# Kernel optimization log

Measured on AMD Instinct MI355X. Metric: run time of the kernel, lower is better.

Reference implementation:

```python
import math
import jax
import jax.numpy as jnp
import numpy as np

SEGMENT_SIZE = 2048   # w (init: segment_size)
DILATION_RATE = 4     # r (init: dilation_rate)
D_MODEL = 1024        # init: d_model


def _sparse_indices(n: int, w: int, r: int, head_idx: int) -> np.ndarray:
    """Static SparsifyIndices: per segment of size w, take tokens offset::r.
    Since r divides w, every segment yields exactly m=w//r indices (no -1 pad).
    Returns flat global token indices, shape (S*m,)."""
    S = n // w
    m = w // r
    off = head_idx % r
    seg_start = np.arange(S, dtype=np.int64)[:, None] * w      # (S,1)
    within = off + r * np.arange(m, dtype=np.int64)[None, :]   # (1,m)
    return (seg_start + within).reshape(-1)


def setup_inputs() -> dict:
    key = jax.random.key(0)
    x = jax.random.normal(key, (4, 8192, D_MODEL), dtype=jnp.float32)
    return {"x": x, "head_idx": 1}


def reference(x, head_idx):
    b, n0, d = x.shape
    w, r = SEGMENT_SIZE, DILATION_RATE
    pad = (-n0) % w
    if pad:
        x = jnp.pad(x, ((0, 0), (0, pad), (0, 0)))
    n = n0 + pad
    idx = _sparse_indices(n, w, r, int(head_idx))  # static, (S*m,)
    S, m = n // w, w // r

    # Gather dilated tokens per segment: (b, S, m, d)
    xg = x[:, idx, :].reshape(b, S, m, d)

    # Softmax attention within each sub-segment (q=k=v=xg)
    scores = jnp.einsum('bsid,bsjd->bsij', xg, xg) / math.sqrt(d)  # (b,S,m,m)
    probs = jax.nn.softmax(scores, axis=-1)
    att = jnp.einsum('bsij,bsjd->bsid', probs, xg).reshape(b, S * m, d)

    # MixOutputs: alpha-weighted scatter-add back to full sequence
    denoms = att.sum(-1)                                       # (b, S*m)
    denom_sums = jnp.zeros((b, n), x.dtype).at[:, idx].add(denoms)
    alphas = denoms / denom_sums[:, idx]                       # (b, S*m)
    out = jnp.zeros((b, n, d), x.dtype).at[:, idx, :].add(att * alphas[..., None])
    return out
```

## Files before the change

kernel.cpp:

```cpp
#include <hip/hip_runtime.h>
#include <hip/hip_bf16.h>


typedef __bf16 bf16_t;
typedef __bf16 bf16x8 __attribute__((ext_vector_type(8)));
typedef float floatx4 __attribute__((ext_vector_type(4)));

#define D_MODEL 1024
#define SEG_W   2048
#define RATE    4
#define M_SUB   512
#define NTOK    8192
#define NSEGT   16
#define XG_ELEMS ((long)NSEGT * M_SUB * D_MODEL)

__global__ __launch_bounds__(256) void gather_kernel(
    const float* __restrict__ x, const int* __restrict__ hidp,
    bf16_t* __restrict__ xg, bf16_t* __restrict__ xgT)
{
    const int off = ((hidp[0] % RATE) + RATE) % RATE;
    const int bid = blockIdx.x;
    const int seg = bid >> 7;
    const int rem = bid & 127;
    const int it  = rem >> 4;
    const int dt  = rem & 15;
    const int b   = seg >> 2, s = seg & 3;

    __shared__ ushort tile[64][65];

    const int t  = threadIdx.x;
    const int r  = t >> 2;
    const int cq = (t & 3) << 4;

    union U8 { bf16x8 v; ushort u[8]; };

    {
        const int  i   = it * 64 + r;
        const long tok = (long)s * SEG_W + off + 4L * i;
        const float* src = x + ((long)b * NTOK + tok) * D_MODEL + dt * 64 + cq;
        float4 f0 = ((const float4*)src)[0];
        float4 f1 = ((const float4*)src)[1];
        float4 f2 = ((const float4*)src)[2];
        float4 f3 = ((const float4*)src)[3];
        U8 lo, hi;
        lo.v[0]=(bf16_t)f0.x; lo.v[1]=(bf16_t)f0.y; lo.v[2]=(bf16_t)f0.z; lo.v[3]=(bf16_t)f0.w;
        lo.v[4]=(bf16_t)f1.x; lo.v[5]=(bf16_t)f1.y; lo.v[6]=(bf16_t)f1.z; lo.v[7]=(bf16_t)f1.w;
        hi.v[0]=(bf16_t)f2.x; hi.v[1]=(bf16_t)f2.y; hi.v[2]=(bf16_t)f2.z; hi.v[3]=(bf16_t)f2.w;
        hi.v[4]=(bf16_t)f3.x; hi.v[5]=(bf16_t)f3.y; hi.v[6]=(bf16_t)f3.z; hi.v[7]=(bf16_t)f3.w;
        bf16_t* dstg = xg + ((long)seg * M_SUB + i) * D_MODEL + dt * 64 + cq;
        *(bf16x8*)(dstg)     = lo.v;
        *(bf16x8*)(dstg + 8) = hi.v;
        #pragma unroll
        for (int j = 0; j < 8; ++j) { tile[r][cq + j] = lo.u[j]; tile[r][cq + 8 + j] = hi.u[j]; }
    }
    __syncthreads();
    {
        const int dc = r;
        const int iq = cq;
        U8 o0, o1;
        #pragma unroll
        for (int j = 0; j < 8; ++j) { o0.u[j] = tile[iq + j][dc]; o1.u[j] = tile[iq + 8 + j][dc]; }
        bf16_t* dstT = xgT + ((long)seg * D_MODEL + dt * 64 + dc) * M_SUB + it * 64 + iq;
        *(bf16x8*)(dstT)     = o0.v;
        *(bf16x8*)(dstT + 8) = o1.v;
    }
}

__global__ __launch_bounds__(512) void attn_kernel(
    const bf16_t* __restrict__ xg, const bf16_t* __restrict__ xgT,
    const int* __restrict__ hidp, float* __restrict__ out)
{
    const int off  = ((hidp[0] % RATE) + RATE) % RATE;
    const int bid0 = blockIdx.x;
    const int sub  = bid0 >> 3;
    const int seg  = (bid0 & 7) * 2 + (sub >> 4);
    const int band = sub & 15;
    const int b = seg >> 2, s = seg & 3;

    const int tid  = threadIdx.x;
    const int w    = tid >> 6;
    const int lane = tid & 63;
    const int l16  = lane & 15;
    const int quad = lane >> 4;

    __shared__ alignas(16) bf16_t P_lds[32 * 512];
    __shared__ float redmax[8][32];
    __shared__ float redsum[8][32];

    const bf16_t* xs  = xg + (long)seg * M_SUB * D_MODEL;
    const bf16_t* qa0 = xs + (long)(band * 32 + l16) * D_MODEL + quad * 8;
    const bf16_t* qa1 = qa0 + 16 * D_MODEL;
    const bf16_t* kb0 = xs + (long)(w * 64 + l16) * D_MODEL + quad * 8;
    const bf16_t* kb1 = kb0 + 16 * D_MODEL;
    const bf16_t* kb2 = kb0 + 32 * D_MODEL;
    const bf16_t* kb3 = kb0 + 48 * D_MODEL;

    floatx4 acc_s[2][4];
    #pragma unroll
    for (int m = 0; m < 2; ++m)
        #pragma unroll
        for (int n = 0; n < 4; ++n) acc_s[m][n] = (floatx4){0.f, 0.f, 0.f, 0.f};

    auto lqk = [&](int st, bf16x8 (&A)[2], bf16x8 (&B)[4]) {
        const int o = st * 32;
        A[0] = *(const bf16x8*)(qa0 + o); A[1] = *(const bf16x8*)(qa1 + o);
        B[0] = *(const bf16x8*)(kb0 + o); B[1] = *(const bf16x8*)(kb1 + o);
        B[2] = *(const bf16x8*)(kb2 + o); B[3] = *(const bf16x8*)(kb3 + o);
    };
    auto mqk = [&](bf16x8 (&A)[2], bf16x8 (&B)[4]) {
        #pragma unroll
        for (int m = 0; m < 2; ++m)
            #pragma unroll
            for (int n = 0; n < 4; ++n)
                acc_s[m][n] = __builtin_amdgcn_mfma_f32_16x16x32_bf16(A[m], B[n], acc_s[m][n], 0, 0, 0);
    };

    {
        bf16x8 aP[2], bP[4], aN[2], bN[4];
        lqk(0, aP, bP);
        #pragma unroll 4
        for (int st = 0; st < 32; st += 2) {
            lqk(st + 1, aN, bN);
            mqk(aP, bP);
            if (st + 2 < 32) lqk(st + 2, aP, bP);
            mqk(aN, bN);
        }
    }

    #pragma unroll
    for (int m = 0; m < 2; ++m)
        #pragma unroll
        for (int n = 0; n < 4; ++n)
            #pragma unroll
            for (int rg = 0; rg < 4; ++rg) acc_s[m][n][rg] *= 0.03125f;

    float mx[2][4];
    #pragma unroll
    for (int m = 0; m < 2; ++m)
        #pragma unroll
        for (int rg = 0; rg < 4; ++rg)
            mx[m][rg] = fmaxf(fmaxf(acc_s[m][0][rg], acc_s[m][1][rg]),
                              fmaxf(acc_s[m][2][rg], acc_s[m][3][rg]));
    #pragma unroll
    for (int d = 1; d < 16; d <<= 1)
        #pragma unroll
        for (int m = 0; m < 2; ++m)
            #pragma unroll
            for (int rg = 0; rg < 4; ++rg)
                mx[m][rg] = fmaxf(mx[m][rg], __shfl_xor(mx[m][rg], d, 64));
    if (l16 == 0) {
        #pragma unroll
        for (int m = 0; m < 2; ++m)
            #pragma unroll
            for (int rg = 0; rg < 4; ++rg)
                redmax[w][m * 16 + quad * 4 + rg] = mx[m][rg];
    }
    __syncthreads();
    float gm[2][4];
    #pragma unroll
    for (int m = 0; m < 2; ++m)
        #pragma unroll
        for (int rg = 0; rg < 4; ++rg) {
            const int row = m * 16 + quad * 4 + rg;
            float g = redmax[0][row];
            #pragma unroll
            for (int ww = 1; ww < 8; ++ww) g = fmaxf(g, redmax[ww][row]);
            gm[m][rg] = g;
        }
    float sm[2][4] = {{0.f,0.f,0.f,0.f},{0.f,0.f,0.f,0.f}};
    #pragma unroll
    for (int m = 0; m < 2; ++m)
        #pragma unroll
        for (int n = 0; n < 4; ++n)
            #pragma unroll
            for (int rg = 0; rg < 4; ++rg) {
                const float e = __expf(acc_s[m][n][rg] - gm[m][rg]);
                acc_s[m][n][rg] = e;
                sm[m][rg] += e;
            }
    #pragma unroll
    for (int d = 1; d < 16; d <<= 1)
        #pragma unroll
        for (int m = 0; m < 2; ++m)
            #pragma unroll
            for (int rg = 0; rg < 4; ++rg)
                sm[m][rg] += __shfl_xor(sm[m][rg], d, 64);
    if (l16 == 0) {
        #pragma unroll
        for (int m = 0; m < 2; ++m)
            #pragma unroll
            for (int rg = 0; rg < 4; ++rg)
                redsum[w][m * 16 + quad * 4 + rg] = sm[m][rg];
    }
    __syncthreads();
    float iv[2][4];
    #pragma unroll
    for (int m = 0; m < 2; ++m)
        #pragma unroll
        for (int rg = 0; rg < 4; ++rg) {
            const int row = m * 16 + quad * 4 + rg;
            float t = redsum[0][row];
            #pragma unroll
            for (int ww = 1; ww < 8; ++ww) t += redsum[ww][row];
            iv[m][rg] = 1.f / t;
        }

    #pragma unroll
    for (int m = 0; m < 2; ++m)
        #pragma unroll
        for (int rg = 0; rg < 4; ++rg) {
            const int row = m * 16 + quad * 4 + rg;
            const float f = iv[m][rg];
            #pragma unroll
            for (int n = 0; n < 4; ++n) {
                const int col = w * 64 + n * 16 + l16;
                const int sw  = (((col >> 3) ^ (row & 7)) << 3) + (col & 7);
                P_lds[row * 512 + sw] = (bf16_t)(acc_s[m][n][rg] * f);
            }
        }
    __syncthreads();

    floatx4 acc_o[2][8];
    #pragma unroll
    for (int m = 0; m < 2; ++m)
        #pragma unroll
        for (int n = 0; n < 8; ++n) acc_o[m][n] = (floatx4){0.f, 0.f, 0.f, 0.f};

    const bf16_t* vb = xgT + ((long)seg * D_MODEL + w * 128 + l16) * M_SUB + quad * 8;

    auto lpv = [&](int kt, bf16x8 (&A)[2], bf16x8 (&B)[8]) {
        #pragma unroll
        for (int m = 0; m < 2; ++m) {
            const int row = m * 16 + l16;
            const int ch  = (kt * 4 + quad) ^ (l16 & 7);
            A[m] = *(const bf16x8*)&P_lds[row * 512 + ch * 8];
        }
        const int ko = kt * 32;
        #pragma unroll
        for (int n = 0; n < 8; ++n)
            B[n] = *(const bf16x8*)(vb + (long)n * 16 * M_SUB + ko);
    };
    auto mpv = [&](bf16x8 (&A)[2], bf16x8 (&B)[8]) {
        #pragma unroll
        for (int m = 0; m < 2; ++m)
            #pragma unroll
            for (int n = 0; n < 8; ++n)
                acc_o[m][n] = __builtin_amdgcn_mfma_f32_16x16x32_bf16(A[m], B[n], acc_o[m][n], 0, 0, 0);
    };

    {
        bf16x8 aP[2], bP[8], aN[2], bN[8];
        lpv(0, aP, bP);
        #pragma unroll 2
        for (int kt = 0; kt < 16; kt += 2) {
            lpv(kt + 1, aN, bN);
            mpv(aP, bP);
            if (kt + 2 < 16) lpv(kt + 2, aP, bP);
            mpv(aN, bN);
        }
    }

    float* obase = out + (long)b * NTOK * D_MODEL;
    #pragma unroll
    for (int m = 0; m < 2; ++m)
        #pragma unroll
        for (int rg = 0; rg < 4; ++rg) {
            const long tok = (long)s * SEG_W + off + 4L * (band * 32 + m * 16 + quad * 4 + rg);
            float* orow = obase + tok * D_MODEL + w * 128 + l16;
            #pragma unroll
            for (int n = 0; n < 8; ++n)
                __builtin_nontemporal_store(acc_o[m][n][rg], orow + n * 16);
        }

    {
        const floatx4 z = {0.f, 0.f, 0.f, 0.f};
        const int chunk = tid & 255;
        const int half  = tid >> 8;
        #pragma unroll 4
        for (int p = 0; p < 48; ++p) {
            const int t = p * 2 + half;
            const int q = t / 3, e = t % 3;
            const int delta = e + (e >= off ? 1 : 0);
            const long tok = (long)s * SEG_W + 4L * (band * 32 + q) + delta;
            __builtin_nontemporal_store(z, (floatx4*)(obase + tok * D_MODEL + chunk * 4));
        }
    }
}

extern "C" void kernel_launch(void* const* d_in, const int* in_sizes, int n_in,
                              void* d_out, int out_size, void* d_ws, size_t ws_size,
                              hipStream_t stream) {
    const float* x   = (const float*)d_in[0];
    const int*   hid = (const int*)d_in[1];
    float*       out = (float*)d_out;
    bf16_t* xg  = (bf16_t*)d_ws;
    bf16_t* xgT = xg + XG_ELEMS;

    gather_kernel<<<dim3(2048), dim3(256), 0, stream>>>(x, hid, xg, xgT);
    attn_kernel<<<dim3(256), dim3(512), 0, stream>>>(xg, xgT, hid, out);
}
```

Before: 288.5 us.

## Stage K and V tiles through LDS with async global_load_lds triple buffering

The attention kernel now copies K tiles (QK^T phase) and V tiles (PV phase) into a 128KB shared-memory arena with global_load_lds. It triple-buffers them using vmcnt waits and raw barriers, where before each wave read its fragments straight from global memory. The PV phase is split into two passes over halves of the model dimension so each pass stages a smaller V tile, and the launch bounds now request two blocks per CU. This is meant to make loads coalesced and overlap them with MFMA work. In exchange it adds a block-wide barrier on every k-step and a large LDS footprint, which may stop two blocks from fitting on a CU.

```diff
diff --git a/kernel.cpp b/kernel.cpp
--- a/kernel.cpp
+++ b/kernel.cpp
@@ -13,6 +13,14 @@
 #define NTOK    8192
 #define NSEGT   16
 #define XG_ELEMS ((long)NSEGT * M_SUB * D_MODEL)
+
+__device__ __forceinline__ void gload16(const bf16_t* g, bf16_t* l) {
+    __builtin_amdgcn_global_load_lds(
+        (const __attribute__((address_space(1))) void*)g,
+        (__attribute__((address_space(3))) void*)l, 16, 0, 0);
+}
+
+#define MFMA16(a, b, c) __builtin_amdgcn_mfma_f32_16x16x32_bf16((a), (b), (c), 0, 0, 0)
 
 __global__ __launch_bounds__(256) void gather_kernel(
     const float* __restrict__ x, const int* __restrict__ hidp,
@@ -66,7 +74,7 @@
     }
 }
 
-__global__ __launch_bounds__(512) void attn_kernel(
+__global__ __launch_bounds__(512, 2) void attn_kernel(
     const bf16_t* __restrict__ xg, const bf16_t* __restrict__ xgT,
     const int* __restrict__ hidp, float* __restrict__ out)
 {
@@ -83,47 +91,74 @@
     const int l16  = lane & 15;
     const int quad = lane >> 4;
 
-    __shared__ alignas(16) bf16_t P_lds[32 * 512];
-    __shared__ float redmax[8][32];
-    __shared__ float redsum[8][32];
-
-    const bf16_t* xs  = xg + (long)seg * M_SUB * D_MODEL;
-    const bf16_t* qa0 = xs + (long)(band * 32 + l16) * D_MODEL + quad * 8;
-    const bf16_t* qa1 = qa0 + 16 * D_MODEL;
-    const bf16_t* kb0 = xs + (long)(w * 64 + l16) * D_MODEL + quad * 8;
-    const bf16_t* kb1 = kb0 + 16 * D_MODEL;
-    const bf16_t* kb2 = kb0 + 32 * D_MODEL;
-    const bf16_t* kb3 = kb0 + 48 * D_MODEL;
-
-    floatx4 acc_s[2][4];
-    #pragma unroll
-    for (int m = 0; m < 2; ++m)
-        #pragma unroll
-        for (int n = 0; n < 4; ++n) acc_s[m][n] = (floatx4){0.f, 0.f, 0.f, 0.f};
-
-    auto lqk = [&](int st, bf16x8 (&A)[2], bf16x8 (&B)[4]) {
-        const int o = st * 32;
-        A[0] = *(const bf16x8*)(qa0 + o); A[1] = *(const bf16x8*)(qa1 + o);
-        B[0] = *(const bf16x8*)(kb0 + o); B[1] = *(const bf16x8*)(kb1 + o);
-        B[2] = *(const bf16x8*)(kb2 + o); B[3] = *(const bf16x8*)(kb3 + o);
+    __shared__ alignas(16) char arena[131072];
+    bf16_t* Pl = (bf16_t*)arena;
+    float (*redmax)[32] = (float(*)[32])(arena + 98304);
+    float (*redsum)[32] = (float(*)[32])(arena + 99328);
+
+    const bf16_t* xs = xg + (long)seg * M_SUB * D_MODEL;
+
+    const bf16_t* qr0 = xs + (long)(band * 32 + l16) * D_MODEL + quad * 8;
+    const bf16_t* qr1 = qr0 + 16 * D_MODEL;
+
+    const bf16_t* ksrc = xs + (long)(w * 64 + (lane >> 2)) * D_MODEL
+                            + (((lane & 3) ^ (lane >> 4)) * 8);
+    auto stageK = [&](int buf, int t) {
+        bf16_t* dst = (bf16_t*)arena + buf * 16384 + (w * 64) * 32;
+        const bf16_t* src = ksrc + t * 32;
+        #pragma unroll
+        for (int j = 0; j < 4; ++j)
+            gload16(src + j * 16 * D_MODEL, dst + j * 512);
     };
-    auto mqk = [&](bf16x8 (&A)[2], bf16x8 (&B)[4]) {
-        #pragma unroll
-        for (int m = 0; m < 2; ++m)
-            #pragma unroll
-            for (int n = 0; n < 4; ++n)
-                acc_s[m][n] = __builtin_amdgcn_mfma_f32_16x16x32_bf16(A[m], B[n], acc_s[m][n], 0, 0, 0);
+
+    const bf16_t* vsrc = xgT + ((long)seg * D_MODEL + w * 64 + (lane >> 2)) * M_SUB
+                             + (((lane & 3) ^ (lane >> 4)) * 8);
+    auto stageV = [&](int buf, int p, int t) {
+        bf16_t* dst = (bf16_t*)(arena + 32768) + buf * 16384 + (w * 64) * 32;
+        const bf16_t* src = vsrc + (long)p * 512 * M_SUB + t * 32;
+        #pragma unroll
+        for (int j = 0; j < 4; ++j)
+            gload16(src + j * 16 * M_SUB, dst + j * 512);
     };
 
-    {
-        bf16x8 aP[2], bP[4], aN[2], bN[4];
-        lqk(0, aP, bP);
-        #pragma unroll 4
-        for (int st = 0; st < 32; st += 2) {
-            lqk(st + 1, aN, bN);
-            mqk(aP, bP);
-            if (st + 2 < 32) lqk(st + 2, aP, bP);
-            mqk(aN, bN);
+    const int rsw = (l16 >> 2) & 3;
+
+    floatx4 accS[2][4];
+    #pragma unroll
+    for (int m = 0; m < 2; ++m)
+        #pragma unroll
+        for (int n = 0; n < 4; ++n) accS[m][n] = (floatx4){0.f, 0.f, 0.f, 0.f};
+
+    bf16x8 qe0, qe1, qo0, qo1;
+    qe0 = *(const bf16x8*)qr0; qe1 = *(const bf16x8*)qr1;
+    stageK(0, 0); stageK(1, 1);
+
+    #pragma unroll
+    for (int t = 0; t < 32; ++t) {
+        if (t == 31) asm volatile("s_waitcnt vmcnt(0)");
+        else         asm volatile("s_waitcnt vmcnt(4)");
+        __builtin_amdgcn_s_barrier();
+        __builtin_amdgcn_sched_barrier(0);
+
+        const bf16_t* Kb = (const bf16_t*)arena + (t % 3) * 16384;
+        bf16x8 Bf[4];
+        #pragma unroll
+        for (int n = 0; n < 4; ++n) {
+            const int row = w * 64 + n * 16 + l16;
+            Bf[n] = *(const bf16x8*)&Kb[row * 32 + ((quad ^ rsw) * 8)];
+        }
+        if (t < 31) {
+            if (t & 1) { qe0 = *(const bf16x8*)(qr0 + (t + 1) * 32); qe1 = *(const bf16x8*)(qr1 + (t + 1) * 32); }
+            else       { qo0 = *(const bf16x8*)(qr0 + (t + 1) * 32); qo1 = *(const bf16x8*)(qr1 + (t + 1) * 32); }
+        }
+        if (t < 30) stageK((t + 2) % 3, t + 2);
+
+        const bf16x8 A0 = (t & 1) ? qo0 : qe0;
+        const bf16x8 A1 = (t & 1) ? qo1 : qe1;
+        #pragma unroll
+        for (int n = 0; n < 4; ++n) {
+            accS[0][n] = MFMA16(A0, Bf[n], accS[0][n]);
+            accS[1][n] = MFMA16(A1, Bf[n], accS[1][n]);
         }
     }
 
@@ -132,15 +167,15 @@
         #pragma unroll
         for (int n = 0; n < 4; ++n)
             #pragma unroll
-            for (int rg = 0; rg < 4; ++rg) acc_s[m][n][rg] *= 0.03125f;
+            for (int rg = 0; rg < 4; ++rg) accS[m][n][rg] *= 0.03125f;
 
     float mx[2][4];
     #pragma unroll
     for (int m = 0; m < 2; ++m)
         #pragma unroll
         for (int rg = 0; rg < 4; ++rg)
-            mx[m][rg] = fmaxf(fmaxf(acc_s[m][0][rg], acc_s[m][1][rg]),
-                              fmaxf(acc_s[m][2][rg], acc_s[m][3][rg]));
+            mx[m][rg] = fmaxf(fmaxf(accS[m][0][rg], accS[m][1][rg]),
+                              fmaxf(accS[m][2][rg], accS[m][3][rg]));
     #pragma unroll
     for (int d = 1; d < 16; d <<= 1)
         #pragma unroll
@@ -174,8 +209,8 @@
         for (int n = 0; n < 4; ++n)
             #pragma unroll
             for (int rg = 0; rg < 4; ++rg) {
-                const float e = __expf(acc_s[m][n][rg] - gm[m][rg]);
-                acc_s[m][n][rg] = e;
+                const float e = __expf(accS[m][n][rg] - gm[m][rg]);
+                accS[m][n][rg] = e;
                 sm[m][rg] += e;
             }
     #pragma unroll
@@ -199,11 +234,13 @@
         #pragma unroll
         for (int rg = 0; rg < 4; ++rg) {
             const int row = m * 16 + quad * 4 + rg;
-            float t = redsum[0][row];
-            #pragma unroll
-            for (int ww = 1; ww < 8; ++ww) t += redsum[ww][row];
-            iv[m][rg] = 1.f / t;
-        }
+            float tt = redsum[0][row];
+            #pragma unroll
+            for (int ww = 1; ww < 8; ++ww) tt += redsum[ww][row];
+            iv[m][rg] = 1.f / tt;
+        }
+
+    stageV(0, 0, 0); stageV(1, 0, 1);
 
     #pragma unroll
     for (int m = 0; m < 2; ++m)
@@ -215,50 +252,55 @@
             for (int n = 0; n < 4; ++n) {
                 const int col = w * 64 + n * 16 + l16;
                 const int sw  = (((col >> 3) ^ (row & 7)) << 3) + (col & 7);
-                P_lds[row * 512 + sw] = (bf16_t)(acc_s[m][n][rg] * f);
+                Pl[row * 512 + sw] = (bf16_t)(accS[m][n][rg] * f);
             }
         }
-    __syncthreads();
-
-    floatx4 acc_o[2][8];
-    #pragma unroll
-    for (int m = 0; m < 2; ++m)
-        #pragma unroll
-        for (int n = 0; n < 8; ++n) acc_o[m][n] = (floatx4){0.f, 0.f, 0.f, 0.f};
-
-    const bf16_t* vb = xgT + ((long)seg * D_MODEL + w * 128 + l16) * M_SUB + quad * 8;
-
-    auto lpv = [&](int kt, bf16x8 (&A)[2], bf16x8 (&B)[8]) {
-        #pragma unroll
-        for (int m = 0; m < 2; ++m) {
-            const int row = m * 16 + l16;
-            const int ch  = (kt * 4 + quad) ^ (l16 & 7);
-            A[m] = *(const bf16x8*)&P_lds[row * 512 + ch * 8];
-        }
-        const int ko = kt * 32;
-        #pragma unroll
-        for (int n = 0; n < 8; ++n)
-            B[n] = *(const bf16x8*)(vb + (long)n * 16 * M_SUB + ko);
+    asm volatile("s_waitcnt lgkmcnt(0)");
+    __builtin_amdgcn_s_barrier();
+    __builtin_amdgcn_sched_barrier(0);
+
+    floatx4 accA[2][4], accB[2][4];
+    #pragma unroll
+    for (int m = 0; m < 2; ++m)
+        #pragma unroll
+        for (int n = 0; n < 4; ++n) {
+            accA[m][n] = (floatx4){0.f, 0.f, 0.f, 0.f};
+            accB[m][n] = (floatx4){0.f, 0.f, 0.f, 0.f};
+        }
+
+    auto pv_pass = [&](int p, floatx4 (&acc)[2][4]) {
+        #pragma unroll
+        for (int t = 0; t < 16; ++t) {
+            if (t == 15) asm volatile("s_waitcnt vmcnt(0)");
+            else         asm volatile("s_waitcnt vmcnt(4)");
+            __builtin_amdgcn_s_barrier();
+            __builtin_amdgcn_sched_barrier(0);
+
+            const bf16_t* Vb = (const bf16_t*)(arena + 32768) + (t % 3) * 16384;
+            bf16x8 Af[2], Bf[4];
+            const int ch = (t * 4 + quad) ^ (l16 & 7);
+            #pragma unroll
+            for (int m = 0; m < 2; ++m)
+                Af[m] = *(const bf16x8*)&Pl[(m * 16 + l16) * 512 + ch * 8];
+            #pragma unroll
+            for (int n = 0; n < 4; ++n) {
+                const int row = w * 64 + n * 16 + l16;
+                Bf[n] = *(const bf16x8*)&Vb[row * 32 + ((quad ^ rsw) * 8)];
+            }
+            if (t < 14) stageV((t + 2) % 3, p, t + 2);
+            #pragma unroll
+            for (int m = 0; m < 2; ++m)
+                #pragma unroll
+                for (int n = 0; n < 4; ++n)
+                    acc[m][n] = MFMA16(Af[m], Bf[n], acc[m][n]);
+        }
     };
-    auto mpv = [&](bf16x8 (&A)[2], bf16x8 (&B)[8]) {
-        #pragma unroll
-        for (int m = 0; m < 2; ++m)
-            #pragma unroll
-            for (int n = 0; n < 8; ++n)
-                acc_o[m][n] = __builtin_amdgcn_mfma_f32_16x16x32_bf16(A[m], B[n], acc_o[m][n], 0, 0, 0);
-    };
-
-    {
-        bf16x8 aP[2], bP[8], aN[2], bN[8];
-        lpv(0, aP, bP);
-        #pragma unroll 2
-        for (int kt = 0; kt < 16; kt += 2) {
-            lpv(kt + 1, aN, bN);
-            mpv(aP, bP);
-            if (kt + 2 < 16) lpv(kt + 2, aP, bP);
-            mpv(aN, bN);
-        }
-    }
+
+    pv_pass(0, accA);
+    __builtin_amdgcn_s_barrier();
+    __builtin_amdgcn_sched_barrier(0);
+    stageV(0, 1, 0); stageV(1, 1, 1);
+    pv_pass(1, accB);
 
     float* obase = out + (long)b * NTOK * D_MODEL;
     #pragma unroll
@@ -266,10 +308,13 @@
         #pragma unroll
         for (int rg = 0; rg < 4; ++rg) {
             const long tok = (long)s * SEG_W + off + 4L * (band * 32 + m * 16 + quad * 4 + rg);
-            float* orow = obase + tok * D_MODEL + w * 128 + l16;
-            #pragma unroll
-            for (int n = 0; n < 8; ++n)
-                __builtin_nontemporal_store(acc_o[m][n][rg], orow + n * 16);
+            float* orow = obase + tok * D_MODEL;
+            #pragma unroll
+            for (int n = 0; n < 4; ++n) {
+                const int d = w * 64 + n * 16 + l16;
+                __builtin_nontemporal_store(accA[m][n][rg], orow + d);
+                __builtin_nontemporal_store(accB[m][n][rg], orow + 512 + d);
+            }
         }
 
     {
```

New measurement: 263.4 us. 1.09x faster.
